# Kernel tuning notes

Measured on AMD Instinct MI355X. Metric: run time of the kernel, lower is better.

## Reference

```python
import jax, jax.numpy as jnp
import numpy as np

N, E, IN, HID, HEADS, OUT = 20000, 320000, 128, 64, 8, 64
NEG_SLOPE = 0.2  # PyG GATConv default leaky_relu slope


def setup_inputs() -> dict:
    key = jax.random.key(0)
    ks = jax.random.split(key, 12)
    g = lambda k, shape, fan_in: jax.random.normal(k, shape, jnp.float32) / np.sqrt(fan_in)
    return {
        "x": jax.random.normal(ks[0], (N, IN), jnp.float32),
        "edge_index": jax.random.randint(ks[1], (2, E), 0, N, jnp.int32),
        "W1": g(ks[2], (IN, HEADS * HID), IN),
        "att_src1": g(ks[3], (HEADS, HID), HID),
        "att_dst1": g(ks[4], (HEADS, HID), HID),
        "b1": jnp.zeros((HEADS * HID,), jnp.float32),
        "W2": g(ks[5], (HEADS * HID, OUT), HEADS * HID),
        "att_src2": g(ks[6], (1, OUT), OUT),
        "att_dst2": g(ks[7], (1, OUT), OUT),
        "b2": jnp.zeros((OUT,), jnp.float32),
    }


def gat_conv(x, edge_index, W, att_src, att_dst, b, heads, out_ch):
    """PyG-style GATConv with add_self_loops=True, concat=True."""
    n = x.shape[0]
    loop = jnp.arange(n, dtype=edge_index.dtype)
    src = jnp.concatenate([edge_index[0], loop])  # message source nodes
    dst = jnp.concatenate([edge_index[1], loop])  # aggregation targets

    h = (x @ W).reshape(n, heads, out_ch)               # [N,H,C]
    a_s = jnp.sum(h * att_src[None], axis=-1)            # [N,H]
    a_d = jnp.sum(h * att_dst[None], axis=-1)            # [N,H]

    e = jax.nn.leaky_relu(a_s[src] + a_d[dst], NEG_SLOPE)  # [Etot,H]
    # numerically stable edge-softmax over incoming neighborhoods
    m = jax.ops.segment_max(e, dst, num_segments=n)
    m = jnp.where(jnp.isfinite(m), m, 0.0)
    p = jnp.exp(e - m[dst])
    denom = jax.ops.segment_sum(p, dst, num_segments=n)
    alpha = p / denom[dst]                               # [Etot,H]

    out = jax.ops.segment_sum(h[src] * alpha[:, :, None], dst, num_segments=n)  # [N,H,C]
    return out.reshape(n, heads * out_ch) + b


def reference(x, edge_index, W1, att_src1, att_dst1, b1, W2, att_src2, att_dst2, b2):
    h = gat_conv(x, edge_index, W1, att_src1, att_dst1, b1, HEADS, HID)
    h = jax.nn.relu(h)
    out = gat_conv(h, edge_index, W2, att_src2, att_dst2, b2, 1, OUT)
    return out
```

## Files before the change

kernel.cpp:

```cpp
#include <hip/hip_runtime.h>
#include <cstdint>

#define N_NODES 20000
#define N_EDGES 320000
#define ET (N_EDGES + N_NODES)
#define IN_DIM 128
#define HID 64
#define HEADS 8
#define F1 (HEADS * HID)
#define OUT_DIM 64
#define NEG_SLOPE 0.2f
#define NB_SCAN 20

typedef __attribute__((ext_vector_type(8))) short bf16x8;
typedef __attribute__((ext_vector_type(4))) float f32x4;

__device__ __forceinline__ ushort f2bf(float f) {
  uint32_t u = __float_as_uint(f);
  uint32_t r = (u + 0x7fffu + ((u >> 16) & 1u)) >> 16;
  return (ushort)r;
}
__device__ __forceinline__ float bfu_lo(uint32_t p) { return __uint_as_float(p << 16); }
__device__ __forceinline__ float bfu_hi(uint32_t p) { return __uint_as_float(p & 0xffff0000u); }
__device__ __forceinline__ float lrelu(float x) { return x > 0.f ? x : NEG_SLOPE * x; }

__global__ void cast_kernel(const float* __restrict__ in, ushort* __restrict__ out, int n4) {
  int i = blockIdx.x * 256 + threadIdx.x;
  if (i >= n4) return;
  float4 v = reinterpret_cast<const float4*>(in)[i];
  ushort4 o;
  o.x = f2bf(v.x); o.y = f2bf(v.y); o.z = f2bf(v.z); o.w = f2bf(v.w);
  reinterpret_cast<ushort4*>(out)[i] = o;
}

__global__ void castT_kernel(const float* __restrict__ in, ushort* __restrict__ out,
                             int R, int C) {
  int idx = blockIdx.x * 256 + threadIdx.x;
  if (idx >= R * C) return;
  int r = idx / C, c = idx - r * C;
  out[(size_t)c * R + r] = f2bf(in[idx]);
}

__global__ void hist_kernel(const int* __restrict__ ei, int* __restrict__ deg) {
  int e = blockIdx.x * 256 + threadIdx.x;
  if (e >= ET) return;
  int dst = (e < N_EDGES) ? ei[N_EDGES + e] : (e - N_EDGES);
  atomicAdd(&deg[dst], 1);
}

__global__ __launch_bounds__(1024) void scan_a(const int* __restrict__ deg,
                                               int* __restrict__ off,
                                               int* __restrict__ bsum) {
  __shared__ int wsum[16];
  int i = blockIdx.x * 1024 + threadIdx.x;
  int lane = threadIdx.x & 63, wid = threadIdx.x >> 6;
  int v = (i < N_NODES) ? deg[i] : 0;
  int s = v;
#pragma unroll
  for (int d = 1; d < 64; d <<= 1) {
    int u = __shfl_up(s, d);
    if (lane >= d) s += u;
  }
  if (lane == 63) wsum[wid] = s;
  __syncthreads();
  if (wid == 0) {
    int ws = (lane < 16) ? wsum[lane] : 0;
#pragma unroll
    for (int d = 1; d < 16; d <<= 1) {
      int u = __shfl_up(ws, d);
      if (lane >= d) ws += u;
    }
    if (lane < 16) wsum[lane] = ws;
  }
  __syncthreads();
  int wbase = (wid > 0) ? wsum[wid - 1] : 0;
  int incl = wbase + s;
  if (i < N_NODES) off[i] = incl - v;
  if (threadIdx.x == 1023) bsum[blockIdx.x] = incl;
}

__global__ void scan_b(const int* __restrict__ bsum, int* __restrict__ boff,
                       int* __restrict__ off) {
  int lane = threadIdx.x;
  int orig = (lane < NB_SCAN) ? bsum[lane] : 0;
  int v = orig;
#pragma unroll
  for (int d = 1; d < 64; d <<= 1) {
    int u = __shfl_up(v, d);
    if (lane >= d) v += u;
  }
  if (lane < NB_SCAN) boff[lane] = v - orig;
  if (lane == NB_SCAN - 1) off[N_NODES] = v;
}

__global__ __launch_bounds__(1024) void scan_c(const int* __restrict__ boff,
                                               int* __restrict__ off,
                                               int* __restrict__ pos) {
  int i = blockIdx.x * 1024 + threadIdx.x;
  if (i >= N_NODES) return;
  int o = off[i] + boff[blockIdx.x];
  off[i] = o;
  pos[i] = o;
}

__global__ void scatter_kernel(const int* __restrict__ ei, int* __restrict__ pos,
                               int* __restrict__ csr_src) {
  int e = blockIdx.x * 256 + threadIdx.x;
  if (e >= ET) return;
  int src, dst;
  if (e < N_EDGES) { src = ei[e]; dst = ei[N_EDGES + e]; }
  else             { src = e - N_EDGES; dst = src; }
  int slot = atomicAdd(&pos[dst], 1);
  csr_src[slot] = src;
}

__device__ __forceinline__ int swz(int r, int kg) { return kg ^ ((r >> 1) & 3); }

template <int WR, int WC, int TM, int TN, int ASD>
__global__ __launch_bounds__(256) void gemm_kernel(
    const ushort* __restrict__ A, const ushort* __restrict__ BT,
    ushort* __restrict__ Cb, int M, int K, int NC,
    const float* __restrict__ atts, const float* __restrict__ attd,
    float* __restrict__ asd) {
  constexpr int BM = WR * TM * 16;
  constexpr int BN = WC * TN * 16;
  __shared__ ushort As[BM * 32];
  __shared__ ushort Bs[BN * 32];
  const int t = threadIdx.x;
  const int lane = t & 63, wid = t >> 6;
  const int wr = wid / WC, wc = wid % WC;
  const int m0 = blockIdx.y * BM, n0 = blockIdx.x * BN;
  f32x4 acc[TM][TN] = {};
  const int srow = t >> 2, kg = t & 3;

  for (int k0 = 0; k0 < K; k0 += 32) {
#pragma unroll
    for (int q = 0; q < BM / 64; ++q) {
      int r = srow + 64 * q;
      int gr = m0 + r; if (gr >= M) gr = M - 1;
      bf16x8 v = *reinterpret_cast<const bf16x8*>(&A[(size_t)gr * K + k0 + kg * 8]);
      *reinterpret_cast<bf16x8*>(&As[r * 32 + swz(r, kg) * 8]) = v;
    }
#pragma unroll
    for (int q = 0; q < BN / 64; ++q) {
      int r = srow + 64 * q;
      int gn = n0 + r;
      bf16x8 v = *reinterpret_cast<const bf16x8*>(&BT[(size_t)gn * K + k0 + kg * 8]);
      *reinterpret_cast<bf16x8*>(&Bs[r * 32 + swz(r, kg) * 8]) = v;
    }
    __syncthreads();
    int kq = lane >> 4;
    int rr = lane & 15;
    bf16x8 af[TM], bfv[TN];
#pragma unroll
    for (int i = 0; i < TM; ++i) {
      int r = (wr * TM + i) * 16 + rr;
      af[i] = *reinterpret_cast<const bf16x8*>(&As[r * 32 + swz(r, kq) * 8]);
    }
#pragma unroll
    for (int j = 0; j < TN; ++j) {
      int r = (wc * TN + j) * 16 + rr;
      bfv[j] = *reinterpret_cast<const bf16x8*>(&Bs[r * 32 + swz(r, kq) * 8]);
    }
#pragma unroll
    for (int i = 0; i < TM; ++i)
#pragma unroll
      for (int j = 0; j < TN; ++j)
        acc[i][j] = __builtin_amdgcn_mfma_f32_16x16x32_bf16(af[i], bfv[j], acc[i][j], 0, 0, 0);
    __syncthreads();
  }
  const int cr0 = (lane >> 4) * 4;
  const int cc = lane & 15;
#pragma unroll
  for (int i = 0; i < TM; ++i)
#pragma unroll
    for (int j = 0; j < TN; ++j)
#pragma unroll
      for (int r = 0; r < 4; ++r) {
        int gm = m0 + (wr * TM + i) * 16 + cr0 + r;
        int gn = n0 + (wc * TN + j) * 16 + cc;
        if (gm < M) Cb[(size_t)gm * NC + gn] = f2bf(acc[i][j][r]);
      }
  if constexpr (ASD != 0) {
    static_assert(TN * 16 == 64, "asd fusion needs 64-col wave tile");
    const int hh = (ASD == 1) ? ((n0 + wc * 64) >> 6) : 0;
    float as_v[TN], ad_v[TN];
#pragma unroll
    for (int j = 0; j < TN; ++j) {
      as_v[j] = atts[hh * 64 + j * 16 + cc];
      ad_v[j] = attd[hh * 64 + j * 16 + cc];
    }
#pragma unroll
    for (int i = 0; i < TM; ++i)
#pragma unroll
      for (int r = 0; r < 4; ++r) {
        float ps = 0.f, pd = 0.f;
#pragma unroll
        for (int j = 0; j < TN; ++j) {
          ps += acc[i][j][r] * as_v[j];
          pd += acc[i][j][r] * ad_v[j];
        }
#pragma unroll
        for (int s = 1; s < 16; s <<= 1) {
          ps += __shfl_xor(ps, s);
          pd += __shfl_xor(pd, s);
        }
        int row = m0 + (wr * TM + i) * 16 + cr0 + r;
        if (cc == 0 && row < M) {
          if constexpr (ASD == 1) {
            asd[(size_t)row * 16 + hh] = ps;
            asd[(size_t)row * 16 + 8 + hh] = pd;
          } else {
            asd[(size_t)row * 2 + 0] = ps;
            asd[(size_t)row * 2 + 1] = pd;
          }
        }
      }
  }
}

template <int H, int ASDS, int DOFF>
__global__ void alpha_kernel(const int* __restrict__ off, const int* __restrict__ csrs,
                             const float* __restrict__ asd, float* __restrict__ alpha) {
  int node = blockIdx.x * 4 + (threadIdx.x >> 6);
  if (node >= N_NODES) return;
  int lane = threadIdx.x & 63;
  int h = lane % H;
  int j = lane / H;
  constexpr int STEP = 64 / H;
  int s0 = off[node], s1 = off[node + 1];
  float adst = asd[(size_t)node * ASDS + DOFF + h];
  float mx = -1e30f;
  for (int i = s0 + j; i < s1; i += STEP) {
    float xv = asd[(size_t)csrs[i] * ASDS + h] + adst;
    mx = fmaxf(mx, lrelu(xv));
  }
#pragma unroll
  for (int s = H; s < 64; s <<= 1) mx = fmaxf(mx, __shfl_xor(mx, s));
  float sum = 0.f;
  for (int i = s0 + j; i < s1; i += STEP) {
    float xv = lrelu(asd[(size_t)csrs[i] * ASDS + h] + adst);
    sum += __expf(xv - mx);
  }
#pragma unroll
  for (int s = H; s < 64; s <<= 1) sum += __shfl_xor(sum, s);
  float inv = 1.f / sum;
  for (int i = s0 + j; i < s1; i += STEP) {
    float xv = lrelu(asd[(size_t)csrs[i] * ASDS + h] + adst);
    alpha[(size_t)i * H + h] = __expf(xv - mx) * inv;
  }
}

__global__ __launch_bounds__(64) void agg1_kernel(
    const int* __restrict__ off, const int* __restrict__ csrs,
    const float* __restrict__ alpha, const ushort* __restrict__ H1b,
    const float* __restrict__ b1, ushort* __restrict__ X2b) {
  int node = blockIdx.x;
  int lane = threadIdx.x;
  int head = lane >> 3;
  int s0 = off[node], s1 = off[node + 1];
  const uint4* Hp = reinterpret_cast<const uint4*>(H1b);
  float a0 = 0.f, a1 = 0.f, a2 = 0.f, a3 = 0.f;
  float a4 = 0.f, a5 = 0.f, a6 = 0.f, a7 = 0.f;
  int i = s0;
  for (; i + 4 <= s1; i += 4) {
    int sA = csrs[i], sB = csrs[i + 1], sC = csrs[i + 2], sD = csrs[i + 3];
    float lA = alpha[(size_t)i * 8 + head];
    float lB = alpha[(size_t)(i + 1) * 8 + head];
    float lC = alpha[(size_t)(i + 2) * 8 + head];
    float lD = alpha[(size_t)(i + 3) * 8 + head];
    uint4 pA = Hp[(size_t)sA * 64 + lane];
    uint4 pB = Hp[(size_t)sB * 64 + lane];
    uint4 pC = Hp[(size_t)sC * 64 + lane];
    uint4 pD = Hp[(size_t)sD * 64 + lane];
    a0 += lA * bfu_lo(pA.x) + lB * bfu_lo(pB.x) + lC * bfu_lo(pC.x) + lD * bfu_lo(pD.x);
    a1 += lA * bfu_hi(pA.x) + lB * bfu_hi(pB.x) + lC * bfu_hi(pC.x) + lD * bfu_hi(pD.x);
    a2 += lA * bfu_lo(pA.y) + lB * bfu_lo(pB.y) + lC * bfu_lo(pC.y) + lD * bfu_lo(pD.y);
    a3 += lA * bfu_hi(pA.y) + lB * bfu_hi(pB.y) + lC * bfu_hi(pC.y) + lD * bfu_hi(pD.y);
    a4 += lA * bfu_lo(pA.z) + lB * bfu_lo(pB.z) + lC * bfu_lo(pC.z) + lD * bfu_lo(pD.z);
    a5 += lA * bfu_hi(pA.z) + lB * bfu_hi(pB.z) + lC * bfu_hi(pC.z) + lD * bfu_hi(pD.z);
    a6 += lA * bfu_lo(pA.w) + lB * bfu_lo(pB.w) + lC * bfu_lo(pC.w) + lD * bfu_lo(pD.w);
    a7 += lA * bfu_hi(pA.w) + lB * bfu_hi(pB.w) + lC * bfu_hi(pC.w) + lD * bfu_hi(pD.w);
  }
  for (; i < s1; ++i) {
    int src = csrs[i];
    float l = alpha[(size_t)i * 8 + head];
    uint4 p = Hp[(size_t)src * 64 + lane];
    a0 += l * bfu_lo(p.x); a1 += l * bfu_hi(p.x);
    a2 += l * bfu_lo(p.y); a3 += l * bfu_hi(p.y);
    a4 += l * bfu_lo(p.z); a5 += l * bfu_hi(p.z);
    a6 += l * bfu_lo(p.w); a7 += l * bfu_hi(p.w);
  }
  float4 bA = reinterpret_cast<const float4*>(b1)[lane * 2];
  float4 bB = reinterpret_cast<const float4*>(b1)[lane * 2 + 1];
  float v0 = fmaxf(a0 + bA.x, 0.f), v1 = fmaxf(a1 + bA.y, 0.f);
  float v2 = fmaxf(a2 + bA.z, 0.f), v3 = fmaxf(a3 + bA.w, 0.f);
  float v4 = fmaxf(a4 + bB.x, 0.f), v5 = fmaxf(a5 + bB.y, 0.f);
  float v6 = fmaxf(a6 + bB.z, 0.f), v7 = fmaxf(a7 + bB.w, 0.f);
  uint4 o;
  o.x = (uint32_t)f2bf(v0) | ((uint32_t)f2bf(v1) << 16);
  o.y = (uint32_t)f2bf(v2) | ((uint32_t)f2bf(v3) << 16);
  o.z = (uint32_t)f2bf(v4) | ((uint32_t)f2bf(v5) << 16);
  o.w = (uint32_t)f2bf(v6) | ((uint32_t)f2bf(v7) << 16);
  reinterpret_cast<uint4*>(X2b)[(size_t)node * 64 + lane] = o;
}

__global__ __launch_bounds__(256) void agg2_kernel(
    const int* __restrict__ off, const int* __restrict__ csrs,
    const float* __restrict__ alpha, const ushort* __restrict__ H2b,
    const float* __restrict__ b2, float* __restrict__ out) {
  int node = blockIdx.x * 4 + (threadIdx.x >> 6);
  if (node >= N_NODES) return;
  int lane = threadIdx.x & 63;
  int grp = lane >> 4, fr = lane & 15;
  int s0 = off[node], s1 = off[node + 1];
  const uint2* Hp = reinterpret_cast<const uint2*>(H2b);
  float a0 = 0.f, a1 = 0.f, a2 = 0.f, a3 = 0.f;
  int i = s0 + grp;
  for (; i + 4 < s1; i += 8) {
    int srcA = csrs[i], srcB = csrs[i + 4];
    float lA = alpha[i], lB = alpha[i + 4];
    uint2 pA = Hp[(size_t)srcA * 16 + fr];
    uint2 pB = Hp[(size_t)srcB * 16 + fr];
    a0 += lA * bfu_lo(pA.x) + lB * bfu_lo(pB.x);
    a1 += lA * bfu_hi(pA.x) + lB * bfu_hi(pB.x);
    a2 += lA * bfu_lo(pA.y) + lB * bfu_lo(pB.y);
    a3 += lA * bfu_hi(pA.y) + lB * bfu_hi(pB.y);
  }
  if (i < s1) {
    int src = csrs[i];
    float l = alpha[i];
    uint2 p = Hp[(size_t)src * 16 + fr];
    a0 += l * bfu_lo(p.x); a1 += l * bfu_hi(p.x);
    a2 += l * bfu_lo(p.y); a3 += l * bfu_hi(p.y);
  }
#pragma unroll
  for (int d = 16; d < 64; d <<= 1) {
    a0 += __shfl_xor(a0, d);
    a1 += __shfl_xor(a1, d);
    a2 += __shfl_xor(a2, d);
    a3 += __shfl_xor(a3, d);
  }
  if (grp == 0) {
    int fb = fr * 4;
    float4 o;
    o.x = a0 + b2[fb];
    o.y = a1 + b2[fb + 1];
    o.z = a2 + b2[fb + 2];
    o.w = a3 + b2[fb + 3];
    reinterpret_cast<float4*>(out)[(size_t)node * 16 + fr] = o;
  }
}

extern "C" void kernel_launch(void* const* d_in, const int* in_sizes, int n_in,
                              void* d_out, int out_size, void* d_ws, size_t ws_size,
                              hipStream_t stream) {
  const float* x        = (const float*)d_in[0];
  const int*   ei       = (const int*)  d_in[1];
  const float* W1       = (const float*)d_in[2];
  const float* att_src1 = (const float*)d_in[3];
  const float* att_dst1 = (const float*)d_in[4];
  const float* b1       = (const float*)d_in[5];
  const float* W2       = (const float*)d_in[6];
  const float* att_src2 = (const float*)d_in[7];
  const float* att_dst2 = (const float*)d_in[8];
  const float* b2       = (const float*)d_in[9];
  float* out = (float*)d_out;

  char* w = (char*)d_ws;
  auto alloc = [&](size_t bytes) {
    char* p = w;
    w += (bytes + 255) & ~(size_t)255;
    return p;
  };
  ushort* xb     = (ushort*)alloc((size_t)N_NODES * IN_DIM * 2);
  ushort* W1T    = (ushort*)alloc((size_t)F1 * IN_DIM * 2);
  ushort* W2T    = (ushort*)alloc((size_t)OUT_DIM * F1 * 2);
  ushort* H1b    = (ushort*)alloc((size_t)N_NODES * F1 * 2);
  ushort* X2b    = (ushort*)alloc((size_t)N_NODES * F1 * 2);
  ushort* H2b    = (ushort*)alloc((size_t)N_NODES * OUT_DIM * 2);
  float* asd1    = (float*)alloc((size_t)N_NODES * 16 * 4);
  float* asd2    = (float*)alloc((size_t)N_NODES * 2 * 4);
  float* alpha1  = (float*)alloc((size_t)ET * 8 * 4);
  float* alpha2  = (float*)alloc((size_t)ET * 4);
  int* deg       = (int*)alloc((size_t)N_NODES * 4);
  int* off       = (int*)alloc((size_t)(N_NODES + 1) * 4);
  int* pos       = (int*)alloc((size_t)N_NODES * 4);
  int* csrsrc    = (int*)alloc((size_t)ET * 4);
  int* bsum      = (int*)alloc((size_t)NB_SCAN * 4);
  int* boff      = (int*)alloc((size_t)NB_SCAN * 4);

  hipMemsetAsync(deg, 0, (size_t)N_NODES * 4, stream);
  hist_kernel<<<(ET + 255) / 256, 256, 0, stream>>>(ei, deg);
  scan_a<<<NB_SCAN, 1024, 0, stream>>>(deg, off, bsum);
  scan_b<<<1, 64, 0, stream>>>(bsum, boff, off);
  scan_c<<<NB_SCAN, 1024, 0, stream>>>(boff, off, pos);
  scatter_kernel<<<(ET + 255) / 256, 256, 0, stream>>>(ei, pos, csrsrc);

  cast_kernel<<<(N_NODES * IN_DIM / 4 + 255) / 256, 256, 0, stream>>>(x, xb, N_NODES * IN_DIM / 4);
  castT_kernel<<<(IN_DIM * F1 + 255) / 256, 256, 0, stream>>>(W1, W1T, IN_DIM, F1);
  castT_kernel<<<(F1 * OUT_DIM + 255) / 256, 256, 0, stream>>>(W2, W2T, F1, OUT_DIM);

  gemm_kernel<2, 2, 4, 4, 1>
      <<<dim3(F1 / 128, (N_NODES + 127) / 128), 256, 0, stream>>>(
      xb, W1T, H1b, N_NODES, IN_DIM, F1, att_src1, att_dst1, asd1);
  alpha_kernel<8, 16, 8><<<(N_NODES + 3) / 4, 256, 0, stream>>>(off, csrsrc, asd1, alpha1);
  agg1_kernel<<<N_NODES, 64, 0, stream>>>(off, csrsrc, alpha1, H1b, b1, X2b);

  gemm_kernel<4, 1, 1, 4, 2>
      <<<dim3(1, (N_NODES + 63) / 64), 256, 0, stream>>>(
      X2b, W2T, H2b, N_NODES, F1, OUT_DIM, att_src2, att_dst2, asd2);
  alpha_kernel<1, 2, 1><<<(N_NODES + 3) / 4, 256, 0, stream>>>(off, csrsrc, asd2, alpha2);
  agg2_kernel<<<(N_NODES + 3) / 4, 256, 0, stream>>>(off, csrsrc, alpha2, H2b, b2, out);
}
```

Measured before the change: 168.1 us.

## Transpose alpha to head-major and split layer-1 aggregation per head

Layer-1 attention weights are now stored head-major, and the layer-1 aggregation launches one wavefront per (head, node) pair instead of one per node. Four lane groups each take a strided share of the edges and combine their partial sums with cross-lane shuffles. The x/W1/W2 cast and transpose kernels are also merged into one prep launch to cut launch count. The aim is more parallelism and contiguous alpha reads, at the cost of re-reading the CSR indices and offsets once per head and making only 8-byte gathers.

```diff
diff --git a/kernel.cpp b/kernel.cpp
--- a/kernel.cpp
+++ b/kernel.cpp
@@ -24,21 +24,25 @@
 __device__ __forceinline__ float bfu_hi(uint32_t p) { return __uint_as_float(p & 0xffff0000u); }
 __device__ __forceinline__ float lrelu(float x) { return x > 0.f ? x : NEG_SLOPE * x; }
 
-__global__ void cast_kernel(const float* __restrict__ in, ushort* __restrict__ out, int n4) {
-  int i = blockIdx.x * 256 + threadIdx.x;
-  if (i >= n4) return;
-  float4 v = reinterpret_cast<const float4*>(in)[i];
-  ushort4 o;
-  o.x = f2bf(v.x); o.y = f2bf(v.y); o.z = f2bf(v.z); o.w = f2bf(v.w);
-  reinterpret_cast<ushort4*>(out)[i] = o;
-}
-
-__global__ void castT_kernel(const float* __restrict__ in, ushort* __restrict__ out,
-                             int R, int C) {
+__global__ void prep_kernel(const float* __restrict__ x, const float* __restrict__ W1,
+                            const float* __restrict__ W2, ushort* __restrict__ xb,
+                            ushort* __restrict__ W1T, ushort* __restrict__ W2T) {
+  const int NX4 = N_NODES * IN_DIM / 4;
   int idx = blockIdx.x * 256 + threadIdx.x;
-  if (idx >= R * C) return;
-  int r = idx / C, c = idx - r * C;
-  out[(size_t)c * R + r] = f2bf(in[idx]);
+  if (idx < NX4) {
+    float4 v = reinterpret_cast<const float4*>(x)[idx];
+    ushort4 o;
+    o.x = f2bf(v.x); o.y = f2bf(v.y); o.z = f2bf(v.z); o.w = f2bf(v.w);
+    reinterpret_cast<ushort4*>(xb)[idx] = o;
+  } else if (idx < NX4 + IN_DIM * F1) {
+    int k = idx - NX4;
+    int r = k / F1, c = k - r * F1;
+    W1T[(size_t)c * IN_DIM + r] = f2bf(W1[k]);
+  } else if (idx < NX4 + IN_DIM * F1 + F1 * OUT_DIM) {
+    int k = idx - NX4 - IN_DIM * F1;
+    int r = k / OUT_DIM, c = k - r * OUT_DIM;
+    W2T[(size_t)c * F1 + r] = f2bf(W2[k]);
+  }
 }
 
 __global__ void hist_kernel(const int* __restrict__ ei, int* __restrict__ deg) {
@@ -247,62 +251,63 @@
   float inv = 1.f / sum;
   for (int i = s0 + j; i < s1; i += STEP) {
     float xv = lrelu(asd[(size_t)csrs[i] * ASDS + h] + adst);
-    alpha[(size_t)i * H + h] = __expf(xv - mx) * inv;
-  }
-}
-
-__global__ __launch_bounds__(64) void agg1_kernel(
+    float a = __expf(xv - mx) * inv;
+    if constexpr (H == 8) alpha[(size_t)h * ET + i] = a;
+    else                  alpha[i] = a;
+  }
+}
+
+__global__ __launch_bounds__(256) void agg1_kernel(
     const int* __restrict__ off, const int* __restrict__ csrs,
-    const float* __restrict__ alpha, const ushort* __restrict__ H1b,
+    const float* __restrict__ alpha,
+    const ushort* __restrict__ H1b,
     const float* __restrict__ b1, ushort* __restrict__ X2b) {
-  int node = blockIdx.x;
-  int lane = threadIdx.x;
-  int head = lane >> 3;
+  int g = blockIdx.x * 4 + (threadIdx.x >> 6);
+  int head = g / N_NODES;
+  int node = g - head * N_NODES;
+  int lane = threadIdx.x & 63;
+  int grp = lane >> 4, fr = lane & 15;
   int s0 = off[node], s1 = off[node + 1];
-  const uint4* Hp = reinterpret_cast<const uint4*>(H1b);
+  const uint2* Hp = reinterpret_cast<const uint2*>(H1b);
+  const float* al = alpha + (size_t)head * ET;
+  const int uoff = head * 16 + fr;
   float a0 = 0.f, a1 = 0.f, a2 = 0.f, a3 = 0.f;
-  float a4 = 0.f, a5 = 0.f, a6 = 0.f, a7 = 0.f;
-  int i = s0;
-  for (; i + 4 <= s1; i += 4) {
-    int sA = csrs[i], sB = csrs[i + 1], sC = csrs[i + 2], sD = csrs[i + 3];
-    float lA = alpha[(size_t)i * 8 + head];
-    float lB = alpha[(size_t)(i + 1) * 8 + head];
-    float lC = alpha[(size_t)(i + 2) * 8 + head];
-    float lD = alpha[(size_t)(i + 3) * 8 + head];
-    uint4 pA = Hp[(size_t)sA * 64 + lane];
-    uint4 pB = Hp[(size_t)sB * 64 + lane];
-    uint4 pC = Hp[(size_t)sC * 64 + lane];
-    uint4 pD = Hp[(size_t)sD * 64 + lane];
-    a0 += lA * bfu_lo(pA.x) + lB * bfu_lo(pB.x) + lC * bfu_lo(pC.x) + lD * bfu_lo(pD.x);
-    a1 += lA * bfu_hi(pA.x) + lB * bfu_hi(pB.x) + lC * bfu_hi(pC.x) + lD * bfu_hi(pD.x);
-    a2 += lA * bfu_lo(pA.y) + lB * bfu_lo(pB.y) + lC * bfu_lo(pC.y) + lD * bfu_lo(pD.y);
-    a3 += lA * bfu_hi(pA.y) + lB * bfu_hi(pB.y) + lC * bfu_hi(pC.y) + lD * bfu_hi(pD.y);
-    a4 += lA * bfu_lo(pA.z) + lB * bfu_lo(pB.z) + lC * bfu_lo(pC.z) + lD * bfu_lo(pD.z);
-    a5 += lA * bfu_hi(pA.z) + lB * bfu_hi(pB.z) + lC * bfu_hi(pC.z) + lD * bfu_hi(pD.z);
-    a6 += lA * bfu_lo(pA.w) + lB * bfu_lo(pB.w) + lC * bfu_lo(pC.w) + lD * bfu_lo(pD.w);
-    a7 += lA * bfu_hi(pA.w) + lB * bfu_hi(pB.w) + lC * bfu_hi(pC.w) + lD * bfu_hi(pD.w);
-  }
-  for (; i < s1; ++i) {
+  int i = s0 + grp;
+  for (; i + 4 < s1; i += 8) {
+    int sA = csrs[i], sB = csrs[i + 4];
+    float lA = al[i], lB = al[i + 4];
+    uint2 pA = Hp[(size_t)sA * 128 + uoff];
+    uint2 pB = Hp[(size_t)sB * 128 + uoff];
+    a0 += lA * bfu_lo(pA.x) + lB * bfu_lo(pB.x);
+    a1 += lA * bfu_hi(pA.x) + lB * bfu_hi(pB.x);
+    a2 += lA * bfu_lo(pA.y) + lB * bfu_lo(pB.y);
+    a3 += lA * bfu_hi(pA.y) + lB * bfu_hi(pB.y);
+  }
+  if (i < s1) {
     int src = csrs[i];
-    float l = alpha[(size_t)i * 8 + head];
-    uint4 p = Hp[(size_t)src * 64 + lane];
+    float l = al[i];
+    uint2 p = Hp[(size_t)src * 128 + uoff];
     a0 += l * bfu_lo(p.x); a1 += l * bfu_hi(p.x);
     a2 += l * bfu_lo(p.y); a3 += l * bfu_hi(p.y);
-    a4 += l * bfu_lo(p.z); a5 += l * bfu_hi(p.z);
-    a6 += l * bfu_lo(p.w); a7 += l * bfu_hi(p.w);
-  }
-  float4 bA = reinterpret_cast<const float4*>(b1)[lane * 2];
-  float4 bB = reinterpret_cast<const float4*>(b1)[lane * 2 + 1];
-  float v0 = fmaxf(a0 + bA.x, 0.f), v1 = fmaxf(a1 + bA.y, 0.f);
-  float v2 = fmaxf(a2 + bA.z, 0.f), v3 = fmaxf(a3 + bA.w, 0.f);
-  float v4 = fmaxf(a4 + bB.x, 0.f), v5 = fmaxf(a5 + bB.y, 0.f);
-  float v6 = fmaxf(a6 + bB.z, 0.f), v7 = fmaxf(a7 + bB.w, 0.f);
-  uint4 o;
-  o.x = (uint32_t)f2bf(v0) | ((uint32_t)f2bf(v1) << 16);
-  o.y = (uint32_t)f2bf(v2) | ((uint32_t)f2bf(v3) << 16);
-  o.z = (uint32_t)f2bf(v4) | ((uint32_t)f2bf(v5) << 16);
-  o.w = (uint32_t)f2bf(v6) | ((uint32_t)f2bf(v7) << 16);
-  reinterpret_cast<uint4*>(X2b)[(size_t)node * 64 + lane] = o;
+  }
+#pragma unroll
+  for (int d = 16; d < 64; d <<= 1) {
+    a0 += __shfl_xor(a0, d);
+    a1 += __shfl_xor(a1, d);
+    a2 += __shfl_xor(a2, d);
+    a3 += __shfl_xor(a3, d);
+  }
+  if (grp == 0) {
+    int fb = head * 64 + fr * 4;
+    float v0 = fmaxf(a0 + b1[fb], 0.f);
+    float v1 = fmaxf(a1 + b1[fb + 1], 0.f);
+    float v2 = fmaxf(a2 + b1[fb + 2], 0.f);
+    float v3 = fmaxf(a3 + b1[fb + 3], 0.f);
+    uint2 o;
+    o.x = (uint32_t)f2bf(v0) | ((uint32_t)f2bf(v1) << 16);
+    o.y = (uint32_t)f2bf(v2) | ((uint32_t)f2bf(v3) << 16);
+    reinterpret_cast<uint2*>(X2b)[(size_t)node * 128 + uoff] = o;
+  }
 }
 
 __global__ __launch_bounds__(256) void agg2_kernel(
@@ -397,15 +402,16 @@
   scan_c<<<NB_SCAN, 1024, 0, stream>>>(boff, off, pos);
   scatter_kernel<<<(ET + 255) / 256, 256, 0, stream>>>(ei, pos, csrsrc);
 
-  cast_kernel<<<(N_NODES * IN_DIM / 4 + 255) / 256, 256, 0, stream>>>(x, xb, N_NODES * IN_DIM / 4);
-  castT_kernel<<<(IN_DIM * F1 + 255) / 256, 256, 0, stream>>>(W1, W1T, IN_DIM, F1);
-  castT_kernel<<<(F1 * OUT_DIM + 255) / 256, 256, 0, stream>>>(W2, W2T, F1, OUT_DIM);
+  {
+    int total = N_NODES * IN_DIM / 4 + IN_DIM * F1 + F1 * OUT_DIM;
+    prep_kernel<<<(total + 255) / 256, 256, 0, stream>>>(x, W1, W2, xb, W1T, W2T);
+  }
 
   gemm_kernel<2, 2, 4, 4, 1>
       <<<dim3(F1 / 128, (N_NODES + 127) / 128), 256, 0, stream>>>(
       xb, W1T, H1b, N_NODES, IN_DIM, F1, att_src1, att_dst1, asd1);
   alpha_kernel<8, 16, 8><<<(N_NODES + 3) / 4, 256, 0, stream>>>(off, csrsrc, asd1, alpha1);
-  agg1_kernel<<<N_NODES, 64, 0, stream>>>(off, csrsrc, alpha1, H1b, b1, X2b);
+  agg1_kernel<<<(HEADS * N_NODES) / 4, 256, 0, stream>>>(off, csrsrc, alpha1, H1b, b1, X2b);
 
   gemm_kernel<4, 1, 1, 4, 2>
       <<<dim3(1, (N_NODES + 63) / 64), 256, 0, stream>>>(
```

Result: slower. 190.2 us (+13.1%).
